# Kernel tuning notes

Hardware: AMD Instinct MI355X
Metric: run time of the kernel (lower is better)

Reference implementation:

```python
import jax, jax.numpy as jnp
import numpy as np

# Model constants (match init_kwargs)
NUM_HEADS = 8
IN_BITS = 64
N_STATE = 256
N_OUT = 64
K_CONN = 8            # n_bits_per_output_neuron
HASH = 65536          # hash_size
K_BITS = 3            # routing key bits
B = 128               # batch of independent sequences
T = 128               # timesteps (windows) per sequence


def setup_inputs() -> dict:
    key = jax.random.key(0)
    k1, k2, k3, k4, k5, k6 = jax.random.split(key, 6)
    # flat bit sequences, split into T windows of IN_BITS in reference()
    bits = jax.random.randint(k1, (B, T * IN_BITS), 0, 2, dtype=jnp.int32)
    # state layer: full connectivity (default n_bits_per_state_neuron =
    # input_bits + n_state_neurons), hashed addressing via random odd-ish
    # integer coefficients dotted with the bit vector, mod HASH.
    total_in = IN_BITS + N_STATE  # 320
    state_coeffs = jax.random.randint(k2, (N_STATE, total_in), 1, HASH, dtype=jnp.int32)
    state_mem = jax.random.uniform(k3, (N_STATE, HASH), dtype=jnp.float32)
    # output heads: each neuron connects to K_CONN random state bits
    head_conn = jax.random.randint(k4, (NUM_HEADS, N_OUT, K_CONN), 0, N_STATE, dtype=jnp.int32)
    head_coeffs = jax.random.randint(k5, (NUM_HEADS, N_OUT, K_CONN), 1, HASH, dtype=jnp.int32)
    head_mem = jax.random.uniform(k6, (NUM_HEADS, N_OUT, HASH), dtype=jnp.float32)
    return {
        "bits": bits,
        "state_coeffs": state_coeffs,
        "state_mem": state_mem,
        "head_conn": head_conn,
        "head_coeffs": head_coeffs,
        "head_mem": head_mem,
    }


def reference(bits, state_coeffs, state_mem, head_conn, head_coeffs, head_mem):
    # windows: [B, T, IN_BITS]
    windows = bits.reshape(B, T, IN_BITS)
    n_state, hash_size = state_mem.shape

    def step(state, w):  # state: [B, N_STATE] int32 bits; w: [B, IN_BITS]
        x = jnp.concatenate([w, state], axis=1)                 # [B, IN+N]
        addr = (x @ state_coeffs.T) % hash_size                 # hashed address [B, N]
        vals = state_mem[jnp.arange(n_state), addr]             # gather [B, N]
        new_state = (vals >= 0.5).astype(jnp.int32)             # RAM output bits
        return new_state, None

    state0 = jnp.zeros((B, n_state), jnp.int32)
    final_state, _ = jax.lax.scan(step, state0, jnp.swapaxes(windows, 0, 1))

    # all output heads read the shared final state
    sel = final_state[:, head_conn]                             # [B, H, O, K]
    addr_h = jnp.einsum('bhok,hok->bho', sel, head_coeffs) % hash_size
    head_vals = head_mem[jnp.arange(NUM_HEADS)[:, None],
                         jnp.arange(N_OUT)[None, :], addr_h]    # [B, H, O]

    # kv routing: pack last K_BITS bits of the final window (MSB first)
    last_w = windows[:, -1, :]
    pow2 = 2 ** jnp.arange(K_BITS - 1, -1, -1)
    head_idx = jnp.sum(last_w[:, -K_BITS:] * pow2, axis=1) % NUM_HEADS  # [B]

    out = head_vals[jnp.arange(B), head_idx]                    # [B, N_OUT]
    return out
```

## Files before the change

### kernel.cpp

```cpp
#include <hip/hip_runtime.h>
#include <stdint.h>

#define T_ 128

typedef int v4i __attribute__((ext_vector_type(4)));

__global__ void prep_bfrag(const int* __restrict__ sc, uint4* __restrict__ bf) {
  int gid = blockIdx.x * 256 + threadIdx.x;
  if (gid >= 160 * 64) return;
  int mf = gid >> 6, l = gid & 63;
  int tau = mf / 10, rem = mf % 10;
  int kap = rem >> 1, h = rem & 1;
  int j = 16 * tau + (l & 15);
  int kinb = (l >> 4) * 16;
  unsigned wout[4];
#pragma unroll
  for (int r = 0; r < 4; ++r) {
    unsigned wrd = 0;
#pragma unroll
    for (int be = 0; be < 4; ++be) {
      int kin = kinb + 4 * r + be;
      int col = (kap == 0) ? kin : 64 + ((kap - 1) << 6) + kin;
      unsigned c = (unsigned)sc[j * 320 + col];
      unsigned byte = (h ? (c >> 8) : c) & 0xFFu;
      byte = (byte - 128u) & 0xFFu;
      wrd |= byte << (8 * be);
    }
    wout[r] = wrd;
  }
  bf[gid] = make_uint4(wout[0], wout[1], wout[2], wout[3]);
}

__global__ void prep_wbits(const int* __restrict__ bits,
                           unsigned long long* __restrict__ wb) {
  int gid = blockIdx.x * 256 + threadIdx.x;
  int wv = gid >> 6, lane = gid & 63;
  unsigned long long m = __ballot(bits[gid] != 0);
  if (lane == 0) wb[wv] = m;
}

__global__ void prep_bitpack(const float* __restrict__ sm,
                             unsigned long long* __restrict__ packed) {
  int base = blockIdx.x * (256 * 32) + threadIdx.x;
  int lane = threadIdx.x & 63;
#pragma unroll 1
  for (int it = 0; it < 32; ++it) {
    int idx = base + it * 256;
    float v = sm[idx];
    unsigned long long m = __ballot(v >= 0.5f);
    if (lane == 0) packed[idx >> 6] = m;
  }
}

__global__ __launch_bounds__(512) void scan_heads(
    const uint4* __restrict__ bfrag,
    const unsigned long long* __restrict__ wbits,
    const unsigned* __restrict__ packed32,
    const int* __restrict__ head_conn,
    const int* __restrict__ head_coeffs,
    const float* __restrict__ head_mem,
    float* __restrict__ out) {
  __shared__ unsigned addrbuf[256];
  __shared__ unsigned long long mshare[4];
  const int tid = threadIdx.x;
  const int b = blockIdx.x;
  const int w = tid >> 6, l = tid & 63;

  v4i bf[2][5][2];
#pragma unroll
  for (int i = 0; i < 2; ++i)
#pragma unroll
    for (int k = 0; k < 5; ++k)
#pragma unroll
      for (int h = 0; h < 2; ++h) {
        int mf = ((2 * w + i) * 5 + k) * 2 + h;
        uint4 u = bfrag[mf * 64 + l];
        bf[i][k][h] = __builtin_bit_cast(v4i, u);
      }

  unsigned long long m0 = 0, m1 = 0, m2 = 0, m3 = 0;
  unsigned long long wcur = wbits[b * 128];
  unsigned NB = (unsigned)__popcll(wcur);

  const int selhi = (l & 32);
  const int sh16 = (l & 16) ? 16 : 0;

#pragma unroll 1
  for (int t = 0; t < T_; ++t) {
    int tn = (t + 1 < T_) ? t + 1 : t;
    unsigned long long wnext = wbits[b * 128 + tn];

    unsigned long long ch0 = wcur, ch1 = m0, ch2 = m1, ch3 = m2, ch4 = m3;
    v4i A[5];
    unsigned long long chs[5] = {ch0, ch1, ch2, ch3, ch4};
#pragma unroll
    for (int c = 0; c < 5; ++c) {
      unsigned lo = (unsigned)chs[c], hi = (unsigned)(chs[c] >> 32);
      unsigned half = selhi ? hi : lo;
      unsigned b16 = (half >> sh16) & 0xFFFFu;
      v4i a;
#pragma unroll
      for (int r = 0; r < 4; ++r) {
        unsigned nib = (b16 >> (4 * r)) & 0xFu;
        a[r] = (int)((nib * 0x00204081u) & 0x01010101u);
      }
      A[c] = a;
    }

    v4i acc00 = (v4i){0, 0, 0, 0}, acc01 = (v4i){0, 0, 0, 0};
    v4i acc10 = (v4i){0, 0, 0, 0}, acc11 = (v4i){0, 0, 0, 0};
#pragma unroll
    for (int k = 0; k < 5; ++k) {
      acc00 = __builtin_amdgcn_mfma_i32_16x16x64_i8(A[k], bf[0][k][0], acc00, 0, 0, 0);
      acc01 = __builtin_amdgcn_mfma_i32_16x16x64_i8(A[k], bf[0][k][1], acc01, 0, 0, 0);
      acc10 = __builtin_amdgcn_mfma_i32_16x16x64_i8(A[k], bf[1][k][0], acc10, 0, 0, 0);
      acc11 = __builtin_amdgcn_mfma_i32_16x16x64_i8(A[k], bf[1][k][1], acc11, 0, 0, 0);
    }

    unsigned corr = (NB * 32896u) & 0xFFFFu;
    unsigned ad0 = ((unsigned)acc00[0] + ((unsigned)acc01[0] << 8) + corr) & 0xFFFFu;
    unsigned ad1 = ((unsigned)acc10[0] + ((unsigned)acc11[0] << 8) + corr) & 0xFFFFu;
    if (l < 16) {
      addrbuf[(2 * w + 0) * 16 + l] = ad0;
      addrbuf[(2 * w + 1) * 16 + l] = ad1;
    }
    __syncthreads();

    if (w < 4) {
      int j2 = (w << 6) + l;
      unsigned ad = addrbuf[j2];
      unsigned word = packed32[((size_t)j2 << 11) + (ad >> 5)];
      unsigned long long mq = __ballot(((word >> (ad & 31)) & 1u) != 0u);
      if (l == 0) mshare[w] = mq;
    }
    __syncthreads();

    m0 = mshare[0]; m1 = mshare[1]; m2 = mshare[2]; m3 = mshare[3];
    NB = (unsigned)(__popcll(m0) + __popcll(m1) + __popcll(m2) +
                    __popcll(m3) + __popcll(wnext));
    wcur = wnext;
  }

  if (w == 0) {
    int h = (int)((((wcur >> 61) & 1) << 2) | (((wcur >> 62) & 1) << 1) |
                  ((wcur >> 63) & 1));
    int ho = h * 64 + l;
    const int4* cn4 = (const int4*)(head_conn + ho * 8);
    const int4* cf4 = (const int4*)(head_coeffs + ho * 8);
    int4 cna = cn4[0], cnb = cn4[1];
    int4 cfa = cf4[0], cfb = cf4[1];
    int cns[8] = {cna.x, cna.y, cna.z, cna.w, cnb.x, cnb.y, cnb.z, cnb.w};
    int cfs[8] = {cfa.x, cfa.y, cfa.z, cfa.w, cfb.x, cfb.y, cfb.z, cfb.w};
    unsigned addr = 0;
#pragma unroll
    for (int k = 0; k < 8; ++k) {
      unsigned bit = (unsigned)((mshare[cns[k] >> 6] >> (cns[k] & 63)) & 1);
      addr += bit * (unsigned)cfs[k];
    }
    addr &= 0xFFFFu;
    out[b * 64 + l] = head_mem[((size_t)ho << 16) + addr];
  }
}

extern "C" void kernel_launch(void* const* d_in, const int* in_sizes, int n_in,
                              void* d_out, int out_size, void* d_ws, size_t ws_size,
                              hipStream_t stream) {
  const int*   bits         = (const int*)d_in[0];
  const int*   state_coeffs = (const int*)d_in[1];
  const float* state_mem    = (const float*)d_in[2];
  const int*   head_conn    = (const int*)d_in[3];
  const int*   head_coeffs  = (const int*)d_in[4];
  const float* head_mem     = (const float*)d_in[5];
  float* out = (float*)d_out;

  char* ws = (char*)d_ws;
  uint4*              bfrag  = (uint4*)ws;
  unsigned long long* wbits  = (unsigned long long*)(ws + (160 << 10));
  unsigned*           packed = (unsigned*)(ws + (288 << 10));

  prep_bfrag<<<40, 256, 0, stream>>>(state_coeffs, bfrag);
  prep_wbits<<<4096, 256, 0, stream>>>(bits, wbits);
  prep_bitpack<<<2048, 256, 0, stream>>>(state_mem, (unsigned long long*)packed);
  scan_heads<<<128, 512, 0, stream>>>(bfrag, wbits, packed,
                                      head_conn, head_coeffs, head_mem, out);
}
```

Baseline: 348.9 us.

## Fuse address gather into all waves, single barrier per step, prefetch input MFMA

Each wave now computes its own 32 state addresses and performs the bit gather directly, removing the LDS address buffer and one of the two barriers per timestep. State bits are exchanged as 32-bit words through a double-buffered shared array. The input-window MFMA contribution for the next step is computed ahead of the barrier, taking it off the serial dependency chain. The per-step recurrence becomes shorter, at the cost of every wave issuing gathers and extra register state.

```diff
diff --git a/kernel.cpp b/kernel.cpp
--- a/kernel.cpp
+++ b/kernel.cpp
@@ -52,6 +52,16 @@
   }
 }
 
+static __device__ __forceinline__ v4i expand16(unsigned b16) {
+  v4i a;
+#pragma unroll
+  for (int r = 0; r < 4; ++r) {
+    unsigned nib = (b16 >> (4 * r)) & 0xFu;
+    a[r] = (int)((nib * 0x00204081u) & 0x01010101u);
+  }
+  return a;
+}
+
 __global__ __launch_bounds__(512) void scan_heads(
     const uint4* __restrict__ bfrag,
     const unsigned long long* __restrict__ wbits,
@@ -60,11 +70,13 @@
     const int* __restrict__ head_coeffs,
     const float* __restrict__ head_mem,
     float* __restrict__ out) {
-  __shared__ unsigned addrbuf[256];
-  __shared__ unsigned long long mshare[4];
+  __shared__ __align__(16) unsigned msh[2][8];
   const int tid = threadIdx.x;
   const int b = blockIdx.x;
   const int w = tid >> 6, l = tid & 63;
+  const int qq = (l >> 4) & 3;
+  const int sh = 16 * (qq & 1);
+  const int wi = qq >> 1;
 
   v4i bf[2][5][2];
 #pragma unroll
@@ -74,70 +86,72 @@
 #pragma unroll
       for (int h = 0; h < 2; ++h) {
         int mf = ((2 * w + i) * 5 + k) * 2 + h;
-        uint4 u = bfrag[mf * 64 + l];
-        bf[i][k][h] = __builtin_bit_cast(v4i, u);
+        bf[i][k][h] = __builtin_bit_cast(v4i, bfrag[mf * 64 + l]);
       }
 
-  unsigned long long m0 = 0, m1 = 0, m2 = 0, m3 = 0;
+  unsigned words[8];
+#pragma unroll
+  for (int i = 0; i < 8; ++i) words[i] = 0u;
   unsigned long long wcur = wbits[b * 128];
-  unsigned NB = (unsigned)__popcll(wcur);
-
-  const int selhi = (l & 32);
-  const int sh16 = (l & 16) ? 16 : 0;
+
+  v4i acc[2][2];
+  {
+    v4i aw = expand16((unsigned)((wcur >> (16 * qq)) & 0xFFFFu));
+    v4i z = (v4i){0, 0, 0, 0};
+#pragma unroll
+    for (int i = 0; i < 2; ++i)
+#pragma unroll
+      for (int h = 0; h < 2; ++h)
+        acc[i][h] = __builtin_amdgcn_mfma_i32_16x16x64_i8(aw, bf[i][0][h], z, 0, 0, 0);
+  }
 
 #pragma unroll 1
   for (int t = 0; t < T_; ++t) {
+    unsigned NB = (unsigned)__popcll(wcur);
+#pragma unroll
+    for (int i = 0; i < 8; ++i) NB += (unsigned)__popc(words[i]);
+
+#pragma unroll
+    for (int c = 0; c < 4; ++c) {
+      v4i a = expand16((words[2 * c + wi] >> sh) & 0xFFFFu);
+      acc[0][0] = __builtin_amdgcn_mfma_i32_16x16x64_i8(a, bf[0][c + 1][0], acc[0][0], 0, 0, 0);
+      acc[0][1] = __builtin_amdgcn_mfma_i32_16x16x64_i8(a, bf[0][c + 1][1], acc[0][1], 0, 0, 0);
+      acc[1][0] = __builtin_amdgcn_mfma_i32_16x16x64_i8(a, bf[1][c + 1][0], acc[1][0], 0, 0, 0);
+      acc[1][1] = __builtin_amdgcn_mfma_i32_16x16x64_i8(a, bf[1][c + 1][1], acc[1][1], 0, 0, 0);
+    }
+
     int tn = (t + 1 < T_) ? t + 1 : t;
     unsigned long long wnext = wbits[b * 128 + tn];
 
-    unsigned long long ch0 = wcur, ch1 = m0, ch2 = m1, ch3 = m2, ch4 = m3;
-    v4i A[5];
-    unsigned long long chs[5] = {ch0, ch1, ch2, ch3, ch4};
-#pragma unroll
-    for (int c = 0; c < 5; ++c) {
-      unsigned lo = (unsigned)chs[c], hi = (unsigned)(chs[c] >> 32);
-      unsigned half = selhi ? hi : lo;
-      unsigned b16 = (half >> sh16) & 0xFFFFu;
-      v4i a;
-#pragma unroll
-      for (int r = 0; r < 4; ++r) {
-        unsigned nib = (b16 >> (4 * r)) & 0xFu;
-        a[r] = (int)((nib * 0x00204081u) & 0x01010101u);
-      }
-      A[c] = a;
-    }
-
-    v4i acc00 = (v4i){0, 0, 0, 0}, acc01 = (v4i){0, 0, 0, 0};
-    v4i acc10 = (v4i){0, 0, 0, 0}, acc11 = (v4i){0, 0, 0, 0};
-#pragma unroll
-    for (int k = 0; k < 5; ++k) {
-      acc00 = __builtin_amdgcn_mfma_i32_16x16x64_i8(A[k], bf[0][k][0], acc00, 0, 0, 0);
-      acc01 = __builtin_amdgcn_mfma_i32_16x16x64_i8(A[k], bf[0][k][1], acc01, 0, 0, 0);
-      acc10 = __builtin_amdgcn_mfma_i32_16x16x64_i8(A[k], bf[1][k][0], acc10, 0, 0, 0);
-      acc11 = __builtin_amdgcn_mfma_i32_16x16x64_i8(A[k], bf[1][k][1], acc11, 0, 0, 0);
-    }
-
     unsigned corr = (NB * 32896u) & 0xFFFFu;
-    unsigned ad0 = ((unsigned)acc00[0] + ((unsigned)acc01[0] << 8) + corr) & 0xFFFFu;
-    unsigned ad1 = ((unsigned)acc10[0] + ((unsigned)acc11[0] << 8) + corr) & 0xFFFFu;
-    if (l < 16) {
-      addrbuf[(2 * w + 0) * 16 + l] = ad0;
-      addrbuf[(2 * w + 1) * 16 + l] = ad1;
-    }
+    unsigned lo = (unsigned)((l & 16) ? acc[1][0][0] : acc[0][0][0]);
+    unsigned hi = (unsigned)((l & 16) ? acc[1][1][0] : acc[0][1][0]);
+    unsigned ad = (lo + (hi << 8) + corr) & 0xFFFFu;
+
+    unsigned bitv = 0;
+    if (l < 32) {
+      unsigned word = packed32[((size_t)(32 * w + l) << 11) + (ad >> 5)];
+      bitv = (word >> (ad & 31)) & 1u;
+    }
+    unsigned long long mq = __ballot(bitv != 0u);
+    if (l == 0) msh[t & 1][w] = (unsigned)mq;
+
+    {
+      v4i aw = expand16((unsigned)((wnext >> (16 * qq)) & 0xFFFFu));
+      v4i z = (v4i){0, 0, 0, 0};
+#pragma unroll
+      for (int i = 0; i < 2; ++i)
+#pragma unroll
+        for (int h = 0; h < 2; ++h)
+          acc[i][h] = __builtin_amdgcn_mfma_i32_16x16x64_i8(aw, bf[i][0][h], z, 0, 0, 0);
+    }
+
     __syncthreads();
 
-    if (w < 4) {
-      int j2 = (w << 6) + l;
-      unsigned ad = addrbuf[j2];
-      unsigned word = packed32[((size_t)j2 << 11) + (ad >> 5)];
-      unsigned long long mq = __ballot(((word >> (ad & 31)) & 1u) != 0u);
-      if (l == 0) mshare[w] = mq;
-    }
-    __syncthreads();
-
-    m0 = mshare[0]; m1 = mshare[1]; m2 = mshare[2]; m3 = mshare[3];
-    NB = (unsigned)(__popcll(m0) + __popcll(m1) + __popcll(m2) +
-                    __popcll(m3) + __popcll(wnext));
+    uint4 u0 = *((const uint4*)&msh[t & 1][0]);
+    uint4 u1 = *((const uint4*)&msh[t & 1][4]);
+    words[0] = u0.x; words[1] = u0.y; words[2] = u0.z; words[3] = u0.w;
+    words[4] = u1.x; words[5] = u1.y; words[6] = u1.z; words[7] = u1.w;
     wcur = wnext;
   }
 
@@ -154,7 +168,7 @@
     unsigned addr = 0;
 #pragma unroll
     for (int k = 0; k < 8; ++k) {
-      unsigned bit = (unsigned)((mshare[cns[k] >> 6] >> (cns[k] & 63)) & 1);
+      unsigned bit = (words[cns[k] >> 5] >> (cns[k] & 31)) & 1u;
       addr += bit * (unsigned)cfs[k];
     }
     addr &= 0xFFFFu;
```

Result: no change. 348.0 us (-0.3%).
